# Kernel tuning notes

Hardware: AMD Instinct MI355X
Metric: run time of the kernel (lower is better)

The kernel has to match this reference:

```python
import jax, jax.numpy as jnp
import numpy as np

B, C, H, W = 4, 256, 64, 64
NHEAD = 8
KH = KW = 3          # partition = [3, 3] -> 9-token windows, stride 1, padding 1
EPS = 1e-5           # torch LayerNorm default


def setup_inputs() -> dict:
    key = jax.random.key(0)
    ks = jax.random.split(key, 3)
    s = 1.0 / np.sqrt(C)  # xavier-ish scale
    return {
        "src": jax.random.normal(ks[0], (B, C, H, W), jnp.float32),
        "ln_w": jnp.ones((C,), jnp.float32),
        "ln_b": jnp.zeros((C,), jnp.float32),
        "in_proj_w": jax.random.normal(ks[1], (3 * C, C), jnp.float32) * s,
        "in_proj_b": jnp.zeros((3 * C,), jnp.float32),
        "out_proj_w": jax.random.normal(ks[2], (C, C), jnp.float32) * s,
        "out_proj_b": jnp.zeros((C,), jnp.float32),
    }


def reference(src, ln_w, ln_b, in_proj_w, in_proj_b, out_proj_w, out_proj_b):
    b, c, h, w = src.shape
    L = h * w
    S = KH * KW  # 9 tokens per local window
    # --- Unfold: overlapping 3x3 windows, padding 1, stride 1 (torch.nn.Unfold order: c major, kernel pos minor)
    xp = jnp.pad(src, ((0, 0), (0, 0), (1, 1), (1, 1)))
    patches = jnp.stack(
        [xp[:, :, i : i + h, j : j + w] for i in range(KH) for j in range(KW)], axis=2
    )  # [b, c, 9, h, w]
    x = patches.reshape(b, c, S, L).transpose(2, 0, 3, 1).reshape(S, b * L, c)  # [S, bL, c]
    # --- Pre-norm (norm1); note: pos embed in the source is overwritten (q = k = src2), FFN is dead code
    mu = x.mean(-1, keepdims=True)
    var = ((x - mu) ** 2).mean(-1, keepdims=True)
    x2 = (x - mu) / jnp.sqrt(var + EPS) * ln_w + ln_b
    # --- MultiheadAttention (self-attn, eval mode -> no dropout)
    qkv = jnp.einsum("sbc,dc->sbd", x2, in_proj_w) + in_proj_b  # [S, bL, 3c]
    q, k, v = jnp.split(qkv, 3, axis=-1)
    dh = c // NHEAD
    scale = dh ** -0.5
    q = q.reshape(S, b * L, NHEAD, dh) * scale
    k = k.reshape(S, b * L, NHEAD, dh)
    v = v.reshape(S, b * L, NHEAD, dh)
    scores = jnp.einsum("sbhd,tbhd->bhst", q, k)        # [bL, H, 9, 9]
    attn = jax.nn.softmax(scores, axis=-1)
    o = jnp.einsum("bhst,tbhd->sbhd", attn, v).reshape(S, b * L, c)
    o = jnp.einsum("sbc,dc->sbd", o, out_proj_w) + out_proj_b
    y = x + o  # residual
    # --- Fold back (kernel 1x1, stride 1): each output pixel = its window's center token
    center = y[S // 2]  # [bL, c]
    return center.reshape(b, L, c).transpose(0, 2, 1).reshape(b, c, h, w)
```

## Files before the change

kernel.cpp:

```cpp
#include <hip/hip_runtime.h>
#include <math.h>


#define NPIX 16384
#define HW   4096
#define CDIM 256

typedef short  bf16x8 __attribute__((ext_vector_type(8)));
typedef float  f32x4  __attribute__((ext_vector_type(4)));
typedef unsigned short u16x8 __attribute__((ext_vector_type(8)));

__device__ inline float bf2f(unsigned short u) {
    unsigned v = ((unsigned)u) << 16;
    return __builtin_bit_cast(float, v);
}
__device__ inline unsigned short f2bf(float f) {
    unsigned u = __builtin_bit_cast(unsigned, f);
    u += 0x7FFFu + ((u >> 16) & 1u);
    return (unsigned short)(u >> 16);
}

__global__ __launch_bounds__(256) void k_prep(const float* __restrict__ Wqkv,
                                              const float* __restrict__ Wout,
                                              const float* __restrict__ bqkv,
                                              const float* __restrict__ lnb,
                                              unsigned short* __restrict__ Wqkvbf,
                                              unsigned short* __restrict__ Woutbf,
                                              float* __restrict__ pads) {
    int bid = blockIdx.x, t = threadIdx.x;
    if (bid < 768) {
        int i = bid * 256 + t;
        Wqkvbf[i] = f2bf(Wqkv[i]);
    } else if (bid < 1024) {
        int i = (bid - 768) * 256 + t;
        Woutbf[i] = f2bf(Wout[i]);
    } else {
        int d = (bid - 1024) * 256 + t;
        int row = 256 + d;
        const float* wrow = Wqkv + (size_t)row * CDIM;
        float s = bqkv[row];
        for (int c = 0; c < CDIM; ++c) s += lnb[c] * wrow[c];
        pads[d] = s;
    }
}

__device__ inline void stageW(const unsigned short* __restrict__ g,
                              unsigned short* lds, int t) {
    int lane = t & 63;
    int wv   = t >> 6;
    int swc  = (lane & 7) ^ ((lane >> 3) & 7);
    #pragma unroll
    for (int it = 0; it < 8; ++it) {
        int rbase = it * 32 + wv * 8;
        const unsigned short* src = g + (size_t)(rbase + (lane >> 3)) * 256 + swc * 8;
        __builtin_amdgcn_global_load_lds(
            (const __attribute__((address_space(1))) void*)src,
            (__attribute__((address_space(3))) void*)(lds + rbase * 64),
            16, 0, 0);
    }
}

__global__ __launch_bounds__(256) void k_ln_qkv(const float* __restrict__ src,
                                                const float* __restrict__ lnw,
                                                const float* __restrict__ lnb,
                                                const unsigned short* __restrict__ Wbf,
                                                const float* __restrict__ bias,
                                                unsigned short* __restrict__ qkvbf) {
    __shared__ unsigned short As[32 * 256];
    __shared__ unsigned short Bs[256 * 64];
    __shared__ float red[8][33];
    __shared__ float red2[8][33];
    __shared__ float muv[32], rsv[32];

    int t = threadIdx.x;
    int bid = blockIdx.x;
    int sb = (bid & 7) * 64 + (bid >> 3);
    int n0 = sb * 32;
    int b = n0 >> 12, p0 = n0 & 4095;

    int pix = t & 31, q = t >> 5;
    const float* sp = src + ((size_t)b * CDIM) * HW + p0 + pix;
    float x[32];
    float sum = 0.f, sq = 0.f;
    #pragma unroll
    for (int i = 0; i < 32; ++i) {
        x[i] = sp[(size_t)(q * 32 + i) * HW];
        sum += x[i]; sq += x[i] * x[i];
    }
    red[q][pix] = sum; red2[q][pix] = sq;
    __syncthreads();
    if (t < 32) {
        float s = 0.f, s2 = 0.f;
        #pragma unroll
        for (int qq = 0; qq < 8; ++qq) { s += red[qq][t]; s2 += red2[qq][t]; }
        float mu = s * (1.f / 256.f);
        float var = fmaxf(s2 * (1.f / 256.f) - mu * mu, 0.f);
        muv[t] = mu; rsv[t] = rsqrtf(var + 1e-5f);
    }
    __syncthreads();
    {
        float mu = muv[pix], rs = rsv[pix];
        #pragma unroll
        for (int c8 = 0; c8 < 4; ++c8) {
            u16x8 o8;
            #pragma unroll
            for (int j = 0; j < 8; ++j) {
                int c = q * 32 + c8 * 8 + j;
                float xn = (x[c8 * 8 + j] - mu) * rs * lnw[c] + lnb[c];
                o8[j] = f2bf(xn);
            }
            int chunk = q * 4 + c8;
            *(u16x8*)((char*)As + (pix * 512 + (((chunk & 7) ^ (pix & 7)) | (chunk & 24)) * 16)) = o8;
        }
    }

    int lane = t & 63, wv = t >> 6;
    int lr = lane & 15, lg = lane >> 4;

    for (int d0 = 0; d0 < 768; d0 += 256) {
        f32x4 acc[2][4] = {};
        for (int k0 = 0; k0 < 256; k0 += 64) {
            __syncthreads();
            stageW(Wbf + (size_t)d0 * 256 + k0, Bs, t);
            __syncthreads();
            #pragma unroll
            for (int kk = 0; kk < 2; ++kk) {
                int chA = (k0 >> 3) + kk * 4 + lg;
                int chB = kk * 4 + lg;
                bf16x8 a[2], bb[4];
                #pragma unroll
                for (int i = 0; i < 2; ++i) {
                    int r = i * 16 + lr;
                    int sl = ((chA & 7) ^ (r & 7)) | (chA & 24);
                    a[i] = *(bf16x8*)((char*)As + (r * 512 + sl * 16));
                }
                #pragma unroll
                for (int j = 0; j < 4; ++j) {
                    int rb = wv * 64 + j * 16 + lr;
                    bb[j] = *(bf16x8*)((char*)Bs + (rb * 128 + ((chB ^ (rb & 7)) * 16)));
                }
                #pragma unroll
                for (int i = 0; i < 2; ++i)
                    #pragma unroll
                    for (int j = 0; j < 4; ++j)
                        acc[i][j] = __builtin_amdgcn_mfma_f32_16x16x32_bf16(
                            a[i], bb[j], acc[i][j], 0, 0, 0);
            }
        }
        unsigned short* Ct = Bs;
        __syncthreads();
        #pragma unroll
        for (int j = 0; j < 4; ++j) {
            float bj = bias[d0 + wv * 64 + j * 16 + lr];
            #pragma unroll
            for (int i = 0; i < 2; ++i)
                #pragma unroll
                for (int r = 0; r < 4; ++r)
                    Ct[(i * 16 + lg * 4 + r) * 264 + wv * 64 + j * 16 + lr] =
                        f2bf(acc[i][j][r] + bj);
        }
        __syncthreads();
        int row = t >> 3, cb = t & 7;
        #pragma unroll
        for (int s = 0; s < 4; ++s) {
            int chunk = cb + 8 * s;
            bf16x8 v = *(bf16x8*)(Ct + row * 264 + chunk * 8);
            *(bf16x8*)(qkvbf + (size_t)(n0 + row) * 768 + d0 + chunk * 8) = v;
        }
    }
}

__global__ __launch_bounds__(256) void k_attn_proj(const unsigned short* __restrict__ qkvbf,
                                                   const float* __restrict__ pads,
                                                   const unsigned short* __restrict__ Wbf,
                                                   const float* __restrict__ bias,
                                                   const float* __restrict__ src,
                                                   float* __restrict__ out) {
    __shared__ unsigned short Bt[32 * 264];
    __shared__ unsigned short As[256 * 64];
    int t  = threadIdx.x;
    int bid = blockIdx.x;
    int sb  = (bid & 7) * 64 + (bid >> 3);
    int n0 = sb * 32;
    int b  = n0 >> 12;
    int p0 = n0 & 4095;

    {
        int pix = t >> 3, h = t & 7;
        int n = n0 + pix;
        int p = n & 4095, hh0 = p >> 6, ww0 = p & 63;
        const float scale = 0.1767766952966369f;

        float qv[32];
        const unsigned short* qp = qkvbf + (size_t)n * 768 + h * 32;
        #pragma unroll
        for (int c8 = 0; c8 < 4; ++c8) {
            bf16x8 v = *(const bf16x8*)(qp + c8 * 8);
            #pragma unroll
            for (int j = 0; j < 8; ++j) qv[c8 * 8 + j] = bf2f((unsigned short)v[j]) * scale;
        }
        float sc[9];
        #pragma unroll
        for (int t9 = 0; t9 < 9; ++t9) {
            int dy = t9 / 3 - 1, dx = t9 % 3 - 1;
            int hh = hh0 + dy, ww = ww0 + dx;
            bool ok = ((unsigned)hh < 64u) && ((unsigned)ww < 64u);
            float a = 0.f;
            if (ok) {
                const unsigned short* kp = qkvbf + (size_t)(n + dy * 64 + dx) * 768 + 256 + h * 32;
                #pragma unroll
                for (int c8 = 0; c8 < 4; ++c8) {
                    bf16x8 v = *(const bf16x8*)(kp + c8 * 8);
                    #pragma unroll
                    for (int j = 0; j < 8; ++j) a += qv[c8 * 8 + j] * bf2f((unsigned short)v[j]);
                }
            } else {
                const float* pk = pads + h * 32;
                #pragma unroll
                for (int j = 0; j < 32; ++j) a += qv[j] * pk[j];
            }
            sc[t9] = a;
        }
        float m = sc[0];
        #pragma unroll
        for (int t9 = 1; t9 < 9; ++t9) m = fmaxf(m, sc[t9]);
        float s = 0.f;
        #pragma unroll
        for (int t9 = 0; t9 < 9; ++t9) { sc[t9] = __expf(sc[t9] - m); s += sc[t9]; }
        float inv = 1.0f / s;

        float ov[32];
        #pragma unroll
        for (int j = 0; j < 32; ++j) ov[j] = 0.f;
        #pragma unroll
        for (int t9 = 0; t9 < 9; ++t9) {
            int dy = t9 / 3 - 1, dx = t9 % 3 - 1;
            int hh = hh0 + dy, ww = ww0 + dx;
            bool ok = ((unsigned)hh < 64u) && ((unsigned)ww < 64u);
            float w = sc[t9] * inv;
            if (ok) {
                const unsigned short* vp = qkvbf + (size_t)(n + dy * 64 + dx) * 768 + 512 + h * 32;
                #pragma unroll
                for (int c8 = 0; c8 < 4; ++c8) {
                    bf16x8 v = *(const bf16x8*)(vp + c8 * 8);
                    #pragma unroll
                    for (int j = 0; j < 8; ++j) ov[c8 * 8 + j] += w * bf2f((unsigned short)v[j]);
                }
            } else {
                const float* pv = pads + 256 + h * 32;
                #pragma unroll
                for (int j = 0; j < 32; ++j) ov[j] += w * pv[j];
            }
        }
        #pragma unroll
        for (int c8 = 0; c8 < 4; ++c8) {
            u16x8 o8;
            #pragma unroll
            for (int j = 0; j < 8; ++j) o8[j] = f2bf(ov[c8 * 8 + j]);
            *(u16x8*)(Bt + pix * 264 + h * 32 + c8 * 8) = o8;
        }
    }
    __syncthreads();

    int lane = t & 63, wv = t >> 6;
    int lr = lane & 15, lg = lane >> 4;
    f32x4 acc[4][2] = {};
    for (int k0 = 0; k0 < 256; k0 += 64) {
        if (k0) __syncthreads();
        stageW(Wbf + k0, As, t);
        __syncthreads();
        #pragma unroll
        for (int kk = 0; kk < 2; ++kk) {
            bf16x8 a[4], bb[2];
            #pragma unroll
            for (int i = 0; i < 4; ++i) {
                int r = wv * 64 + i * 16 + lr;
                int sl = (kk * 4 + lg) ^ (r & 7);
                a[i] = *(bf16x8*)((char*)As + (r * 128 + sl * 16));
            }
            #pragma unroll
            for (int j = 0; j < 2; ++j)
                bb[j] = *(bf16x8*)(Bt + (j * 16 + lr) * 264 + k0 + kk * 32 + lg * 8);
            #pragma unroll
            for (int i = 0; i < 4; ++i)
                #pragma unroll
                for (int j = 0; j < 2; ++j)
                    acc[i][j] = __builtin_amdgcn_mfma_f32_16x16x32_bf16(
                        a[i], bb[j], acc[i][j], 0, 0, 0);
        }
    }
    #pragma unroll
    for (int i = 0; i < 4; ++i) {
        #pragma unroll
        for (int r = 0; r < 4; ++r) {
            int dg = wv * 64 + i * 16 + lg * 4 + r;
            float bd = bias[dg];
            #pragma unroll
            for (int j = 0; j < 2; ++j) {
                int ng = p0 + j * 16 + lr;
                size_t idx = ((size_t)(b * CDIM + dg)) * HW + ng;
                out[idx] = acc[i][j][r] + bd + src[idx];
            }
        }
    }
}

extern "C" void kernel_launch(void* const* d_in, const int* in_sizes, int n_in,
                              void* d_out, int out_size, void* d_ws, size_t ws_size,
                              hipStream_t stream) {
    const float* src  = (const float*)d_in[0];
    const float* lnw  = (const float*)d_in[1];
    const float* lnb  = (const float*)d_in[2];
    const float* Wqkv = (const float*)d_in[3];
    const float* bqkv = (const float*)d_in[4];
    const float* Wout = (const float*)d_in[5];
    const float* bout = (const float*)d_in[6];
    float* out = (float*)d_out;

    unsigned short* qkvbf  = (unsigned short*)d_ws;
    unsigned short* Wqkvbf = qkvbf + (size_t)NPIX * 768;
    unsigned short* Woutbf = Wqkvbf + 768 * 256;
    float* pads = (float*)(Woutbf + 256 * 256);

    k_prep<<<1026, 256, 0, stream>>>(Wqkv, Wout, bqkv, lnb, Wqkvbf, Woutbf, pads);
    k_ln_qkv<<<512, 256, 0, stream>>>(src, lnw, lnb, Wqkvbf, bqkv, qkvbf);
    k_attn_proj<<<512, 256, 0, stream>>>(qkvbf, pads, Woutbf, bout, src, out);
}
```

Before: 55.28 us.

## Double-buffer weight staging in 32-wide K chunks to overlap loads with MFMA

Both GEMM kernels now stage weights in 32-column K chunks into two LDS buffers. The next chunk is prefetched with global_load_lds while the current one feeds the MFMAs, so each chunk needs one barrier instead of two. The first chunk is issued at kernel start so it overlaps the LayerNorm and attention prologues. The LN reduction scratch and the output transpose buffer are aliased into the second weight buffer, with a swizzled layout, to keep LDS use about the same. The price is more barriers overall with smaller chunks, and correctness now relies on the barrier also waiting for the outstanding async LDS loads.

New measurement: 58.55 us. +5.9%, slower.

```diff
diff --git a/kernel.cpp b/kernel.cpp
--- a/kernel.cpp
+++ b/kernel.cpp
@@ -44,18 +44,20 @@
     }
 }
 
-__device__ inline void stageW(const unsigned short* __restrict__ g,
-                              unsigned short* lds, int t) {
+__device__ inline void stageW32(const unsigned short* __restrict__ g,
+                                unsigned short* lds, int t) {
     int lane = t & 63;
     int wv   = t >> 6;
-    int swc  = (lane & 7) ^ ((lane >> 3) & 7);
+    int rin  = lane >> 2;
+    int slot = lane & 3;
     #pragma unroll
-    for (int it = 0; it < 8; ++it) {
-        int rbase = it * 32 + wv * 8;
-        const unsigned short* src = g + (size_t)(rbase + (lane >> 3)) * 256 + swc * 8;
+    for (int it = 0; it < 4; ++it) {
+        int rbase = (wv * 4 + it) * 16;
+        int row = rbase + rin;
+        const unsigned short* src = g + (size_t)row * 256 + ((slot ^ (row & 3)) * 8);
         __builtin_amdgcn_global_load_lds(
             (const __attribute__((address_space(1))) void*)src,
-            (__attribute__((address_space(3))) void*)(lds + rbase * 64),
+            (__attribute__((address_space(3))) void*)(lds + rbase * 32),
             16, 0, 0);
     }
 }
@@ -67,10 +69,7 @@
                                                 const float* __restrict__ bias,
                                                 unsigned short* __restrict__ qkvbf) {
     __shared__ unsigned short As[32 * 256];
-    __shared__ unsigned short Bs[256 * 64];
-    __shared__ float red[8][33];
-    __shared__ float red2[8][33];
-    __shared__ float muv[32], rsv[32];
+    __shared__ unsigned short Bs[2][256 * 32];
 
     int t = threadIdx.x;
     int bid = blockIdx.x;
@@ -78,6 +77,12 @@
     int n0 = sb * 32;
     int b = n0 >> 12, p0 = n0 & 4095;
 
+    stageW32(Wbf, Bs[0], t);
+
+    float* red  = (float*)(&Bs[1][0]);
+    float* red2 = red + 264;
+    float* muv  = red + 528;
+    float* rsv  = red + 560;
     int pix = t & 31, q = t >> 5;
     const float* sp = src + ((size_t)b * CDIM) * HW + p0 + pix;
     float x[32];
@@ -87,12 +92,12 @@
         x[i] = sp[(size_t)(q * 32 + i) * HW];
         sum += x[i]; sq += x[i] * x[i];
     }
-    red[q][pix] = sum; red2[q][pix] = sq;
+    red[q * 33 + pix] = sum; red2[q * 33 + pix] = sq;
     __syncthreads();
     if (t < 32) {
         float s = 0.f, s2 = 0.f;
         #pragma unroll
-        for (int qq = 0; qq < 8; ++qq) { s += red[qq][t]; s2 += red2[qq][t]; }
+        for (int qq = 0; qq < 8; ++qq) { s += red[qq * 33 + t]; s2 += red2[qq * 33 + t]; }
         float mu = s * (1.f / 256.f);
         float var = fmaxf(s2 * (1.f / 256.f) - mu * mu, 0.f);
         muv[t] = mu; rsv[t] = rsqrtf(var + 1e-5f);
@@ -113,60 +118,69 @@
             *(u16x8*)((char*)As + (pix * 512 + (((chunk & 7) ^ (pix & 7)) | (chunk & 24)) * 16)) = o8;
         }
     }
+    __syncthreads();
 
     int lane = t & 63, wv = t >> 6;
     int lr = lane & 15, lg = lane >> 4;
 
-    for (int d0 = 0; d0 < 768; d0 += 256) {
+    for (int pass = 0; pass < 3; ++pass) {
         f32x4 acc[2][4] = {};
-        for (int k0 = 0; k0 < 256; k0 += 64) {
+        #pragma unroll
+        for (int kc = 0; kc < 8; ++kc) {
+            int s = pass * 8 + kc;
+            if (s < 23) {
+                int ns = s + 1;
+                stageW32(Wbf + (size_t)((ns >> 3) * 256) * 256 + (ns & 7) * 32,
+                         Bs[ns & 1], t);
+            }
+            const unsigned short* B = Bs[s & 1];
+            int chA = kc * 4 + lg;
+            bf16x8 a[2], bb[4];
+            #pragma unroll
+            for (int i = 0; i < 2; ++i) {
+                int r = i * 16 + lr;
+                int sl = ((chA & 7) ^ (r & 7)) | (chA & 24);
+                a[i] = *(bf16x8*)((char*)As + (r * 512 + sl * 16));
+            }
+            #pragma unroll
+            for (int j = 0; j < 4; ++j) {
+                int rb = wv * 64 + j * 16 + lr;
+                bb[j] = *(bf16x8*)((char*)B + (rb * 64 + ((lg ^ (rb & 3)) * 16)));
+            }
+            #pragma unroll
+            for (int i = 0; i < 2; ++i)
+                #pragma unroll
+                for (int j = 0; j < 4; ++j)
+                    acc[i][j] = __builtin_amdgcn_mfma_f32_16x16x32_bf16(
+                        a[i], bb[j], acc[i][j], 0, 0, 0);
             __syncthreads();
-            stageW(Wbf + (size_t)d0 * 256 + k0, Bs, t);
-            __syncthreads();
-            #pragma unroll
-            for (int kk = 0; kk < 2; ++kk) {
-                int chA = (k0 >> 3) + kk * 4 + lg;
-                int chB = kk * 4 + lg;
-                bf16x8 a[2], bb[4];
-                #pragma unroll
-                for (int i = 0; i < 2; ++i) {
-                    int r = i * 16 + lr;
-                    int sl = ((chA & 7) ^ (r & 7)) | (chA & 24);
-                    a[i] = *(bf16x8*)((char*)As + (r * 512 + sl * 16));
-                }
-                #pragma unroll
-                for (int j = 0; j < 4; ++j) {
-                    int rb = wv * 64 + j * 16 + lr;
-                    bb[j] = *(bf16x8*)((char*)Bs + (rb * 128 + ((chB ^ (rb & 7)) * 16)));
-                }
-                #pragma unroll
-                for (int i = 0; i < 2; ++i)
-                    #pragma unroll
-                    for (int j = 0; j < 4; ++j)
-                        acc[i][j] = __builtin_amdgcn_mfma_f32_16x16x32_bf16(
-                            a[i], bb[j], acc[i][j], 0, 0, 0);
-            }
-        }
-        unsigned short* Ct = Bs;
-        __syncthreads();
+        }
+        int d0 = pass * 256;
+        unsigned short* Ct = (unsigned short*)Bs[1];
         #pragma unroll
         for (int j = 0; j < 4; ++j) {
             float bj = bias[d0 + wv * 64 + j * 16 + lr];
             #pragma unroll
             for (int i = 0; i < 2; ++i)
                 #pragma unroll
-                for (int r = 0; r < 4; ++r)
-                    Ct[(i * 16 + lg * 4 + r) * 264 + wv * 64 + j * 16 + lr] =
-                        f2bf(acc[i][j][r] + bj);
+                for (int r2 = 0; r2 < 4; ++r2) {
+                    int row = i * 16 + lg * 4 + r2;
+                    int col = wv * 64 + j * 16 + lr;
+                    int chunk = col >> 3;
+                    int sl = ((chunk & 7) ^ (row & 7)) | (chunk & 24);
+                    Ct[row * 256 + sl * 8 + (col & 7)] = f2bf(acc[i][j][r2] + bj);
+                }
         }
         __syncthreads();
         int row = t >> 3, cb = t & 7;
         #pragma unroll
-        for (int s = 0; s < 4; ++s) {
-            int chunk = cb + 8 * s;
-            bf16x8 v = *(bf16x8*)(Ct + row * 264 + chunk * 8);
+        for (int s2 = 0; s2 < 4; ++s2) {
+            int chunk = cb + 8 * s2;
+            int sl = ((chunk & 7) ^ (row & 7)) | (chunk & 24);
+            bf16x8 v = *(bf16x8*)(Ct + row * 256 + sl * 8);
             *(bf16x8*)(qkvbf + (size_t)(n0 + row) * 768 + d0 + chunk * 8) = v;
         }
+        __syncthreads();
     }
 }
 
@@ -177,13 +191,15 @@
                                                    const float* __restrict__ src,
                                                    float* __restrict__ out) {
     __shared__ unsigned short Bt[32 * 264];
-    __shared__ unsigned short As[256 * 64];
+    __shared__ unsigned short As2[2][256 * 32];
     int t  = threadIdx.x;
     int bid = blockIdx.x;
     int sb  = (bid & 7) * 64 + (bid >> 3);
     int n0 = sb * 32;
     int b  = n0 >> 12;
     int p0 = n0 & 4095;
+
+    stageW32(Wbf, As2[0], t);
 
     {
         int pix = t >> 3, h = t & 7;
@@ -265,41 +281,38 @@
     int lane = t & 63, wv = t >> 6;
     int lr = lane & 15, lg = lane >> 4;
     f32x4 acc[4][2] = {};
-    for (int k0 = 0; k0 < 256; k0 += 64) {
-        if (k0) __syncthreads();
-        stageW(Wbf + k0, As, t);
+    #pragma unroll
+    for (int kc = 0; kc < 8; ++kc) {
+        if (kc < 7) stageW32(Wbf + (kc + 1) * 32, As2[(kc + 1) & 1], t);
+        const unsigned short* A = As2[kc & 1];
+        bf16x8 a[4], bb[2];
+        #pragma unroll
+        for (int i = 0; i < 4; ++i) {
+            int r = wv * 64 + i * 16 + lr;
+            a[i] = *(bf16x8*)((char*)A + (r * 64 + ((lg ^ (r & 3)) * 16)));
+        }
+        #pragma unroll
+        for (int j = 0; j < 2; ++j)
+            bb[j] = *(bf16x8*)(Bt + (j * 16 + lr) * 264 + kc * 32 + lg * 8);
+        #pragma unroll
+        for (int i = 0; i < 4; ++i)
+            #pragma unroll
+            for (int j = 0; j < 2; ++j)
+                acc[i][j] = __builtin_amdgcn_mfma_f32_16x16x32_bf16(
+                    a[i], bb[j], acc[i][j], 0, 0, 0);
         __syncthreads();
-        #pragma unroll
-        for (int kk = 0; kk < 2; ++kk) {
-            bf16x8 a[4], bb[2];
-            #pragma unroll
-            for (int i = 0; i < 4; ++i) {
-                int r = wv * 64 + i * 16 + lr;
-                int sl = (kk * 4 + lg) ^ (r & 7);
-                a[i] = *(bf16x8*)((char*)As + (r * 128 + sl * 16));
-            }
-            #pragma unroll
-            for (int j = 0; j < 2; ++j)
-                bb[j] = *(bf16x8*)(Bt + (j * 16 + lr) * 264 + k0 + kk * 32 + lg * 8);
-            #pragma unroll
-            for (int i = 0; i < 4; ++i)
-                #pragma unroll
-                for (int j = 0; j < 2; ++j)
-                    acc[i][j] = __builtin_amdgcn_mfma_f32_16x16x32_bf16(
-                        a[i], bb[j], acc[i][j], 0, 0, 0);
-        }
     }
     #pragma unroll
     for (int i = 0; i < 4; ++i) {
         #pragma unroll
-        for (int r = 0; r < 4; ++r) {
-            int dg = wv * 64 + i * 16 + lg * 4 + r;
+        for (int r2 = 0; r2 < 4; ++r2) {
+            int dg = wv * 64 + i * 16 + lg * 4 + r2;
             float bd = bias[dg];
             #pragma unroll
             for (int j = 0; j < 2; ++j) {
                 int ng = p0 + j * 16 + lr;
                 size_t idx = ((size_t)(b * CDIM + dg)) * HW + ng;
-                out[idx] = acc[i][j][r] + bd + src[idx];
+                out[idx] = acc[i][j][r2] + bd + src[idx];
             }
         }
     }
```
